# Optimization experiments

Hardware: AMD Instinct MI355X
Metric: run time of the kernel (lower is better)

## Reference

```python
import jax, jax.numpy as jnp
import numpy as np

B = 262144
DIM = 128
TD = 32        # token_dim (per-token channel dim inside attention)
NT = DIM // TD # 4 tokens from x, +1 learnable -> N = 5
N = NT + 1
H = 8          # num_heads
HD = TD // H   # head_dim = 4
DEEP = 2


def setup_inputs() -> dict:
    key = jax.random.key(0)
    ks = jax.random.split(key, 7)
    x = jax.random.normal(ks[0], (B, DIM), dtype=jnp.float32)
    token = jax.random.normal(ks[1], (1, 1, TD), dtype=jnp.float32)
    # stacked per-layer params (DEEP layers)
    qkv_w = jax.random.normal(ks[2], (DEEP, 3 * TD, TD), dtype=jnp.float32) * (TD ** -0.5)
    qkv_b = jnp.zeros((DEEP, 3 * TD), dtype=jnp.float32)
    proj_w = jax.random.normal(ks[3], (DEEP, TD, TD), dtype=jnp.float32) * (TD ** -0.5)
    proj_b = jnp.zeros((DEEP, TD), dtype=jnp.float32)
    pos_bias = jax.random.normal(ks[4], (DEEP, H, N, N), dtype=jnp.float32)
    return {"x": x, "token": token, "qkv_w": qkv_w, "qkv_b": qkv_b,
            "proj_w": proj_w, "proj_b": proj_b, "pos_bias": pos_bias}


def reference(x, token, qkv_w, qkv_b, proj_w, proj_b, pos_bias):
    scale = HD ** -0.5
    b = x.shape[0]
    # split x into NT tokens of width TD, prepend learnable token -> [B, N, TD]
    y = jnp.concatenate(
        [jnp.broadcast_to(token, (b, 1, TD)), x.reshape(b, NT, TD)], axis=1)
    for i in range(DEEP):
        qkv = y @ qkv_w[i].T + qkv_b[i]                 # [B, N, 3*TD]
        qkv = qkv.reshape(b, N, 3, H, HD)
        q = qkv[:, :, 0].transpose(0, 2, 1, 3)          # [B, H, N, HD]
        k = qkv[:, :, 1].transpose(0, 2, 1, 3)
        v = qkv[:, :, 2].transpose(0, 2, 1, 3)
        attn = jnp.einsum('bhnd,bhmd->bhnm', q, k) * scale + pos_bias[i]
        attn = jax.nn.softmax(attn, axis=-1)
        o = jnp.einsum('bhnm,bhmd->bhnd', attn, v)      # [B, H, N, HD]
        o = o.transpose(0, 2, 1, 3).reshape(b, N, TD)
        y = y + (o @ proj_w[i].T + proj_b[i])           # residual
    return y[:, 0, :]                                   # [B, TD]
```

## Files before the change

kernel.cpp:

```cpp
#include <hip/hip_runtime.h>
#include <hip/hip_bf16.h>


#define NTOK 5

typedef decltype(__builtin_amdgcn_cvt_pkrtz(0.0f, 0.0f)) half2_t;
using half8_t = __attribute__((ext_vector_type(8))) _Float16;
using f32x4 = __attribute__((ext_vector_type(4))) float;
using f32x2 = __attribute__((ext_vector_type(2))) float;

union H2 { half2_t h; unsigned int u; };
union H8 { half8_t h; uint4 u4; unsigned int u[4]; };

__device__ __forceinline__ half2_t u2h(unsigned int x) { H2 c; c.u = x; return c.h; }
__device__ __forceinline__ unsigned int h2u(half2_t h) { H2 c; c.h = h; return c.u; }
__device__ __forceinline__ unsigned int pk(float a, float b) {
  return h2u(__builtin_amdgcn_cvt_pkrtz(a, b));
}
__device__ __forceinline__ float bf2f(unsigned short u) {
  union { unsigned int u; float f; } c; c.u = ((unsigned int)u) << 16; return c.f;
}
__device__ __forceinline__ half2_t bfpair2h2(unsigned int u) {
  union { unsigned int u; float f; } lo, hi;
  lo.u = u << 16;
  hi.u = u & 0xffff0000u;
  return __builtin_amdgcn_cvt_pkrtz(lo.f, hi.f);
}
__device__ __forceinline__ unsigned int f2bfpair(float a, float b) {
  unsigned int ua = __float_as_uint(a), ub = __float_as_uint(b);
  ua = (ua + 0x7fffu + ((ua >> 16) & 1u)) >> 16;
  ub = (ub + 0x7fffu + ((ub >> 16) & 1u)) & 0xffff0000u;
  return ua | ub;
}

__device__ __forceinline__ int detect_bf16(const unsigned int* __restrict__ p) {
  int cnt = 0;
#pragma unroll
  for (int i = 0; i < 64; ++i) {
    unsigned int e = (p[i] >> 7) & 0xffu;
    cnt += (e >= 96u && e <= 150u) ? 1 : 0;
  }
  return (cnt >= 40) ? 1 : 0;
}

__device__ __forceinline__ int permch(int pos) {
  return 4 * (pos >> 3) + (pos & 3) + ((pos & 4) ? 16 : 0);
}

__global__ void prep_kernel(const void* __restrict__ xraw,
                            const void* __restrict__ qkv_w, const void* __restrict__ qkv_b,
                            const void* __restrict__ proj_w, const void* __restrict__ proj_b,
                            const void* __restrict__ pos_b,
                            unsigned int* __restrict__ wqkv, unsigned int* __restrict__ wproj,
                            float* __restrict__ bqkv, float* __restrict__ bproj,
                            float* __restrict__ pb, int* __restrict__ flag) {
  const int t = threadIdx.x;
  const int isbf = detect_bf16((const unsigned int*)xraw);
  if (t == 0) *flag = isbf;
  const float LOG2E = 1.44269504f;
  if (isbf) {
    const unsigned short* qw = (const unsigned short*)qkv_w;
    const unsigned short* qb = (const unsigned short*)qkv_b;
    const unsigned short* pw = (const unsigned short*)proj_w;
    const unsigned short* pbb = (const unsigned short*)proj_b;
    const unsigned short* pp = (const unsigned short*)pos_b;
    for (int i = t; i < 3072; i += 256) {
      const int row = i >> 4, cp = (i & 15) * 2;
      wqkv[i] = h2u(__builtin_amdgcn_cvt_pkrtz(bf2f(qw[row * 32 + permch(cp)]),
                                               bf2f(qw[row * 32 + permch(cp + 1)])));
    }
    for (int i = t; i < 1024; i += 256) {
      const int row = i >> 4, cp = (i & 15) * 2;
      wproj[i] = h2u(__builtin_amdgcn_cvt_pkrtz(bf2f(pw[row * 32 + permch(cp)]),
                                                bf2f(pw[row * 32 + permch(cp + 1)])));
    }
    for (int i = t; i < 192; i += 256) bqkv[i] = bf2f(qb[i]);
    for (int i = t; i < 64; i += 256) bproj[i] = bf2f(pbb[i]);
    for (int i = t; i < 640; i += 256) {
      const int m = i & 7, r = i >> 3;
      const int n = r % 5, lh = r / 5;
      pb[i] = (m < 5) ? bf2f(pp[lh * 25 + n * 5 + m]) * LOG2E : 0.0f;
    }
  } else {
    const float* qw = (const float*)qkv_w;
    const float* qb = (const float*)qkv_b;
    const float* pw = (const float*)proj_w;
    const float* pbb = (const float*)proj_b;
    const float* pp = (const float*)pos_b;
    for (int i = t; i < 3072; i += 256) {
      const int row = i >> 4, cp = (i & 15) * 2;
      wqkv[i] = h2u(__builtin_amdgcn_cvt_pkrtz(qw[row * 32 + permch(cp)],
                                               qw[row * 32 + permch(cp + 1)]));
    }
    for (int i = t; i < 1024; i += 256) {
      const int row = i >> 4, cp = (i & 15) * 2;
      wproj[i] = h2u(__builtin_amdgcn_cvt_pkrtz(pw[row * 32 + permch(cp)],
                                                pw[row * 32 + permch(cp + 1)]));
    }
    for (int i = t; i < 192; i += 256) bqkv[i] = qb[i];
    for (int i = t; i < 64; i += 256) bproj[i] = pbb[i];
    for (int i = t; i < 640; i += 256) {
      const int m = i & 7, r = i >> 3;
      const int n = r % 5, lh = r / 5;
      pb[i] = (m < 5) ? pp[lh * 25 + n * 5 + m] * LOG2E : 0.0f;
    }
  }
}

__device__ __forceinline__ half8_t mk8(const unsigned int (&d)[4]) {
  H8 c; c.u[0] = d[0]; c.u[1] = d[1]; c.u[2] = d[2]; c.u[3] = d[3]; return c.h;
}

__device__ __forceinline__ half8_t ldsfrag(const unsigned int* lw, int row, int quad) {
  H8 c; c.u4 = *(const uint4*)(lw + row * 20 + quad * 4); return c.h;
}

template <int NR>
__device__ __forceinline__ void attn_head(const unsigned int (&qd)[NR][2],
                                          const unsigned int (&kd)[NTOK][2],
                                          const f32x4 (&vv)[NTOK],
                                          const float* pbh,
                                          unsigned int (&od)[NR][2]) {
#pragma unroll
  for (int n = 0; n < NR; ++n) {
    const f32x4 pbv = *(const f32x4*)(pbh + n * 8);
    const float pb4 = pbh[n * 8 + 4];
    const float pbm[NTOK] = {pbv[0], pbv[1], pbv[2], pbv[3], pb4};
    const half2_t q0 = u2h(qd[n][0]), q1 = u2h(qd[n][1]);
    float e[NTOK];
#pragma unroll
    for (int m = 0; m < NTOK; ++m) {
      float d = __builtin_amdgcn_fdot2(q0, u2h(kd[m][0]), 0.0f, false);
      d = __builtin_amdgcn_fdot2(q1, u2h(kd[m][1]), d, false);
      e[m] = __builtin_amdgcn_exp2f(fmaf(d, 0.72134752f, pbm[m]));
    }
    const float ssum = ((e[0] + e[1]) + (e[2] + e[3])) + e[4];
    const float r = __builtin_amdgcn_rcpf(ssum);
    f32x2 o01 = {0.0f, 0.0f}, o23 = {0.0f, 0.0f};
#pragma unroll
    for (int m = 0; m < NTOK; ++m) {
      const f32x2 em = {e[m], e[m]};
      const f32x2 vlo = {vv[m][0], vv[m][1]};
      const f32x2 vhi = {vv[m][2], vv[m][3]};
      o01 = __builtin_elementwise_fma(em, vlo, o01);
      o23 = __builtin_elementwise_fma(em, vhi, o23);
    }
    od[n][0] = pk(o01[0] * r, o01[1] * r);
    od[n][1] = pk(o23[0] * r, o23[1] * r);
  }
}

__global__ __launch_bounds__(256, 4) void vit_kernel(
    const void* __restrict__ x, const void* __restrict__ token,
    const unsigned int* __restrict__ wqkv, const unsigned int* __restrict__ wproj,
    const float* __restrict__ bqkv, const float* __restrict__ bproj,
    const float* __restrict__ pb, const int* __restrict__ flag,
    void* __restrict__ out) {
  __shared__ unsigned int lds_w[256 * 20];
  __shared__ float lds_bq[192];
  __shared__ float lds_bp[64];
  __shared__ float lds_pb[640];

  const int tid = threadIdx.x;
  const int wave = tid >> 6, lane = tid & 63;
  const int quad = lane >> 4, nl = lane & 15;
  const size_t b = (size_t)blockIdx.x * 64 + wave * 16 + nl;
  const int isbf = *flag;

  uint2 xb16[10];
  float4 xf32[10];
  if (isbf) {
    const unsigned short* tk = (const unsigned short*)token;
    xb16[0] = *(const uint2*)(tk + quad * 4);
    xb16[1] = *(const uint2*)(tk + quad * 4 + 16);
    const unsigned short* xbp = (const unsigned short*)x + b * 128;
#pragma unroll
    for (int t = 1; t < NTOK; ++t) {
      const unsigned short* base = xbp + (t - 1) * 32;
      xb16[2 * t] = *(const uint2*)(base + quad * 4);
      xb16[2 * t + 1] = *(const uint2*)(base + quad * 4 + 16);
    }
  } else {
    const float* tk = (const float*)token;
    xf32[0] = *(const float4*)(tk + quad * 4);
    xf32[1] = *(const float4*)(tk + quad * 4 + 16);
    const float* xbp = (const float*)x + b * 128;
#pragma unroll
    for (int t = 1; t < NTOK; ++t) {
      const float* base = xbp + (t - 1) * 32;
      xf32[2 * t] = *(const float4*)(base + quad * 4);
      xf32[2 * t + 1] = *(const float4*)(base + quad * 4 + 16);
    }
  }

  {
    const uint4* sq = (const uint4*)wqkv;
#pragma unroll
    for (int k = 0; k < 3; ++k) {
      const int i = tid + k * 256;
      *(uint4*)(lds_w + (i >> 2) * 20 + (i & 3) * 4) = sq[i];
    }
    const uint4* sp = (const uint4*)wproj;
    *(uint4*)(lds_w + (192 + (tid >> 2)) * 20 + (tid & 3) * 4) = sp[tid];
    if (tid < 192) lds_bq[tid] = bqkv[tid];
    if (tid < 64) lds_bp[tid] = bproj[tid];
    {
      const uint4* spb = (const uint4*)pb;
      if (tid < 160) *(uint4*)((float*)lds_pb + tid * 4) = spb[tid];
    }
  }
  __syncthreads();

  unsigned int yd[NTOK][4];
  if (isbf) {
#pragma unroll
    for (int t = 0; t < NTOK; ++t) {
      yd[t][0] = h2u(bfpair2h2(xb16[2 * t].x));
      yd[t][1] = h2u(bfpair2h2(xb16[2 * t].y));
      yd[t][2] = h2u(bfpair2h2(xb16[2 * t + 1].x));
      yd[t][3] = h2u(bfpair2h2(xb16[2 * t + 1].y));
    }
  } else {
#pragma unroll
    for (int t = 0; t < NTOK; ++t) {
      yd[t][0] = pk(xf32[2 * t].x, xf32[2 * t].y);
      yd[t][1] = pk(xf32[2 * t].z, xf32[2 * t].w);
      yd[t][2] = pk(xf32[2 * t + 1].x, xf32[2 * t + 1].y);
      yd[t][3] = pk(xf32[2 * t + 1].z, xf32[2 * t + 1].w);
    }
  }

  unsigned int od[2][NTOK][2];
#pragma unroll
  for (int s = 0; s < 2; ++s) {
    const half8_t waq = ldsfrag(lds_w, (s) * 16 + nl, quad);
    const half8_t wak = ldsfrag(lds_w, (2 + s) * 16 + nl, quad);
    const half8_t wav = ldsfrag(lds_w, (4 + s) * 16 + nl, quad);
    const f32x4 bq = *(const f32x4*)(lds_bq + (s) * 16 + quad * 4);
    const f32x4 bk = *(const f32x4*)(lds_bq + (2 + s) * 16 + quad * 4);
    const f32x4 bv = *(const f32x4*)(lds_bq + (4 + s) * 16 + quad * 4);
    unsigned int qd[NTOK][2], kd[NTOK][2];
    f32x4 vv[NTOK];
#pragma unroll
    for (int t = 0; t < NTOK; ++t) {
      const half8_t yb = mk8(yd[t]);
      const f32x4 aq = __builtin_amdgcn_mfma_f32_16x16x32_f16(waq, yb, bq, 0, 0, 0);
      qd[t][0] = pk(aq[0], aq[1]); qd[t][1] = pk(aq[2], aq[3]);
      const f32x4 ak = __builtin_amdgcn_mfma_f32_16x16x32_f16(wak, yb, bk, 0, 0, 0);
      kd[t][0] = pk(ak[0], ak[1]); kd[t][1] = pk(ak[2], ak[3]);
      vv[t] = __builtin_amdgcn_mfma_f32_16x16x32_f16(wav, yb, bv, 0, 0, 0);
    }
    attn_head<NTOK>(qd, kd, vv, lds_pb + (quad + 4 * s) * 40, od[s]);
  }

  {
    half8_t wp[2]; f32x4 bp[2];
#pragma unroll
    for (int tile = 0; tile < 2; ++tile) {
      wp[tile] = ldsfrag(lds_w, 192 + tile * 16 + nl, quad);
      bp[tile] = *(const f32x4*)(lds_bp + tile * 16 + quad * 4);
    }
#pragma unroll
    for (int t = 0; t < NTOK; ++t) {
      unsigned int bfr[4] = {od[0][t][0], od[0][t][1], od[1][t][0], od[1][t][1]};
      const half8_t ob = mk8(bfr);
      f32x4 p0 = __builtin_amdgcn_mfma_f32_16x16x32_f16(wp[0], ob, bp[0], 0, 0, 0);
      f32x4 p1 = __builtin_amdgcn_mfma_f32_16x16x32_f16(wp[1], ob, bp[1], 0, 0, 0);
      yd[t][0] = h2u(u2h(yd[t][0]) + u2h(pk(p0[0], p0[1])));
      yd[t][1] = h2u(u2h(yd[t][1]) + u2h(pk(p0[2], p0[3])));
      yd[t][2] = h2u(u2h(yd[t][2]) + u2h(pk(p1[0], p1[1])));
      yd[t][3] = h2u(u2h(yd[t][3]) + u2h(pk(p1[2], p1[3])));
    }
  }

  unsigned int o1[2][1][2];
#pragma unroll
  for (int s = 0; s < 2; ++s) {
    const half8_t waq = ldsfrag(lds_w, 96 + (s) * 16 + nl, quad);
    const half8_t wak = ldsfrag(lds_w, 96 + (2 + s) * 16 + nl, quad);
    const half8_t wav = ldsfrag(lds_w, 96 + (4 + s) * 16 + nl, quad);
    const f32x4 bq = *(const f32x4*)(lds_bq + 96 + (s) * 16 + quad * 4);
    const f32x4 bk = *(const f32x4*)(lds_bq + 96 + (2 + s) * 16 + quad * 4);
    const f32x4 bv = *(const f32x4*)(lds_bq + 96 + (4 + s) * 16 + quad * 4);
    unsigned int qd[1][2], kd[NTOK][2];
    f32x4 vv[NTOK];
    {
      const f32x4 aq = __builtin_amdgcn_mfma_f32_16x16x32_f16(waq, mk8(yd[0]), bq, 0, 0, 0);
      qd[0][0] = pk(aq[0], aq[1]); qd[0][1] = pk(aq[2], aq[3]);
    }
#pragma unroll
    for (int t = 0; t < NTOK; ++t) {
      const half8_t yb = mk8(yd[t]);
      const f32x4 ak = __builtin_amdgcn_mfma_f32_16x16x32_f16(wak, yb, bk, 0, 0, 0);
      kd[t][0] = pk(ak[0], ak[1]); kd[t][1] = pk(ak[2], ak[3]);
      vv[t] = __builtin_amdgcn_mfma_f32_16x16x32_f16(wav, yb, bv, 0, 0, 0);
    }
    attn_head<1>(qd, kd, vv, lds_pb + (8 + quad + 4 * s) * 40, o1[s]);
  }

  {
    half8_t wp[2]; f32x4 bp[2];
#pragma unroll
    for (int tile = 0; tile < 2; ++tile) {
      wp[tile] = ldsfrag(lds_w, 192 + 32 + tile * 16 + nl, quad);
      bp[tile] = *(const f32x4*)(lds_bp + 32 + tile * 16 + quad * 4);
    }
    unsigned int bfr[4] = {o1[0][0][0], o1[0][0][1], o1[1][0][0], o1[1][0][1]};
    const half8_t ob = mk8(bfr);
    f32x4 p0 = __builtin_amdgcn_mfma_f32_16x16x32_f16(wp[0], ob, bp[0], 0, 0, 0);
    f32x4 p1 = __builtin_amdgcn_mfma_f32_16x16x32_f16(wp[1], ob, bp[1], 0, 0, 0);

    const half2_t y0 = u2h(yd[0][0]), y1 = u2h(yd[0][1]);
    const half2_t y2 = u2h(yd[0][2]), y3 = u2h(yd[0][3]);
    float f[8] = {(float)y0.x + p0[0], (float)y0.y + p0[1],
                  (float)y1.x + p0[2], (float)y1.y + p0[3],
                  (float)y2.x + p1[0], (float)y2.y + p1[1],
                  (float)y3.x + p1[2], (float)y3.y + p1[3]};
    if (isbf) {
      unsigned short* ob16 = (unsigned short*)out + b * 32;
      *(uint2*)(ob16 + quad * 4) = make_uint2(f2bfpair(f[0], f[1]), f2bfpair(f[2], f[3]));
      *(uint2*)(ob16 + quad * 4 + 16) = make_uint2(f2bfpair(f[4], f[5]), f2bfpair(f[6], f[7]));
    } else {
      float* of = (float*)out + b * 32;
      *(float4*)(of + quad * 4) = make_float4(f[0], f[1], f[2], f[3]);
      *(float4*)(of + quad * 4 + 16) = make_float4(f[4], f[5], f[6], f[7]);
    }
  }
}

extern "C" void kernel_launch(void* const* d_in, const int* in_sizes, int n_in,
                              void* d_out, int out_size, void* d_ws, size_t ws_size,
                              hipStream_t stream) {
  const void* x      = d_in[0];
  const void* token  = d_in[1];
  const void* qkv_w  = d_in[2];
  const void* qkv_b  = d_in[3];
  const void* proj_w = d_in[4];
  const void* proj_b = d_in[5];
  const void* pos_b  = d_in[6];

  char* ws = (char*)d_ws;
  unsigned int* wqkv  = (unsigned int*)(ws + 0);
  unsigned int* wproj = (unsigned int*)(ws + 12288);
  float* bqkv  = (float*)(ws + 16384);
  float* bproj = (float*)(ws + 17152);
  float* pb    = (float*)(ws + 17408);
  int*   flag  = (int*)(ws + 19968);

  prep_kernel<<<1, 256, 0, stream>>>(x, qkv_w, qkv_b, proj_w, proj_b, pos_b,
                                     wqkv, wproj, bqkv, bproj, pb, flag);

  const int nrows = in_sizes[0] / 128;
  const int grid = nrows / 64;
  vit_kernel<<<grid, 256, 0, stream>>>(x, token, wqkv, wproj, bqkv, bproj, pb, flag, d_out);
}
```

Measured before the change: 232.9 us.

## Process four row groups per block with register prefetch of next inputs

Each block now loops over four 64-row groups. The LDS weight, bias and position-bias setup is paid once per block instead of once per 64 rows, and the x loads for the next group are issued before the current group's compute so memory latency overlaps MFMA work. Launch bounds drop from 4 to 3 blocks per SIMD to leave registers for the prefetch buffers, and the grid shrinks fourfold. The risks are lower occupancy, more register pressure, and an uneven tail over the smaller grid; the last iteration also issues a redundant reload.

```diff
diff --git a/kernel.cpp b/kernel.cpp
--- a/kernel.cpp
+++ b/kernel.cpp
@@ -150,7 +150,9 @@
   }
 }
 
-__global__ __launch_bounds__(256, 4) void vit_kernel(
+#define NITER 4
+
+__global__ __launch_bounds__(256, 3) void vit_kernel(
     const void* __restrict__ x, const void* __restrict__ token,
     const unsigned int* __restrict__ wqkv, const unsigned int* __restrict__ wproj,
     const float* __restrict__ bqkv, const float* __restrict__ bproj,
@@ -164,32 +166,27 @@
   const int tid = threadIdx.x;
   const int wave = tid >> 6, lane = tid & 63;
   const int quad = lane >> 4, nl = lane & 15;
-  const size_t b = (size_t)blockIdx.x * 64 + wave * 16 + nl;
+  const int rowoff = wave * 16 + nl;
+  const size_t bbase = (size_t)blockIdx.x * (64 * NITER) + rowoff;
   const int isbf = *flag;
 
-  uint2 xb16[10];
-  float4 xf32[10];
+  float4 rawf[8];
+  uint2 rawb[8];
   if (isbf) {
-    const unsigned short* tk = (const unsigned short*)token;
-    xb16[0] = *(const uint2*)(tk + quad * 4);
-    xb16[1] = *(const uint2*)(tk + quad * 4 + 16);
-    const unsigned short* xbp = (const unsigned short*)x + b * 128;
+    const unsigned short* xbp = (const unsigned short*)x + bbase * 128;
 #pragma unroll
     for (int t = 1; t < NTOK; ++t) {
       const unsigned short* base = xbp + (t - 1) * 32;
-      xb16[2 * t] = *(const uint2*)(base + quad * 4);
-      xb16[2 * t + 1] = *(const uint2*)(base + quad * 4 + 16);
+      rawb[2 * (t - 1)] = *(const uint2*)(base + quad * 4);
+      rawb[2 * (t - 1) + 1] = *(const uint2*)(base + quad * 4 + 16);
     }
   } else {
-    const float* tk = (const float*)token;
-    xf32[0] = *(const float4*)(tk + quad * 4);
-    xf32[1] = *(const float4*)(tk + quad * 4 + 16);
-    const float* xbp = (const float*)x + b * 128;
+    const float* xbp = (const float*)x + bbase * 128;
 #pragma unroll
     for (int t = 1; t < NTOK; ++t) {
       const float* base = xbp + (t - 1) * 32;
-      xf32[2 * t] = *(const float4*)(base + quad * 4);
-      xf32[2 * t + 1] = *(const float4*)(base + quad * 4 + 16);
+      rawf[2 * (t - 1)] = *(const float4*)(base + quad * 4);
+      rawf[2 * (t - 1) + 1] = *(const float4*)(base + quad * 4 + 16);
     }
   }
 
@@ -209,121 +206,164 @@
       if (tid < 160) *(uint4*)((float*)lds_pb + tid * 4) = spb[tid];
     }
   }
+
+  unsigned int tokd[4];
+  if (isbf) {
+    const unsigned short* tk = (const unsigned short*)token;
+    const uint2 t0 = *(const uint2*)(tk + quad * 4);
+    const uint2 t1 = *(const uint2*)(tk + quad * 4 + 16);
+    tokd[0] = h2u(bfpair2h2(t0.x)); tokd[1] = h2u(bfpair2h2(t0.y));
+    tokd[2] = h2u(bfpair2h2(t1.x)); tokd[3] = h2u(bfpair2h2(t1.y));
+  } else {
+    const float* tk = (const float*)token;
+    const float4 a0 = *(const float4*)(tk + quad * 4);
+    const float4 a1 = *(const float4*)(tk + quad * 4 + 16);
+    tokd[0] = pk(a0.x, a0.y); tokd[1] = pk(a0.z, a0.w);
+    tokd[2] = pk(a1.x, a1.y); tokd[3] = pk(a1.z, a1.w);
+  }
   __syncthreads();
 
-  unsigned int yd[NTOK][4];
-  if (isbf) {
-#pragma unroll
-    for (int t = 0; t < NTOK; ++t) {
-      yd[t][0] = h2u(bfpair2h2(xb16[2 * t].x));
-      yd[t][1] = h2u(bfpair2h2(xb16[2 * t].y));
-      yd[t][2] = h2u(bfpair2h2(xb16[2 * t + 1].x));
-      yd[t][3] = h2u(bfpair2h2(xb16[2 * t + 1].y));
-    }
-  } else {
-#pragma unroll
-    for (int t = 0; t < NTOK; ++t) {
-      yd[t][0] = pk(xf32[2 * t].x, xf32[2 * t].y);
-      yd[t][1] = pk(xf32[2 * t].z, xf32[2 * t].w);
-      yd[t][2] = pk(xf32[2 * t + 1].x, xf32[2 * t + 1].y);
-      yd[t][3] = pk(xf32[2 * t + 1].z, xf32[2 * t + 1].w);
-    }
-  }
-
-  unsigned int od[2][NTOK][2];
-#pragma unroll
-  for (int s = 0; s < 2; ++s) {
-    const half8_t waq = ldsfrag(lds_w, (s) * 16 + nl, quad);
-    const half8_t wak = ldsfrag(lds_w, (2 + s) * 16 + nl, quad);
-    const half8_t wav = ldsfrag(lds_w, (4 + s) * 16 + nl, quad);
-    const f32x4 bq = *(const f32x4*)(lds_bq + (s) * 16 + quad * 4);
-    const f32x4 bk = *(const f32x4*)(lds_bq + (2 + s) * 16 + quad * 4);
-    const f32x4 bv = *(const f32x4*)(lds_bq + (4 + s) * 16 + quad * 4);
-    unsigned int qd[NTOK][2], kd[NTOK][2];
-    f32x4 vv[NTOK];
-#pragma unroll
-    for (int t = 0; t < NTOK; ++t) {
-      const half8_t yb = mk8(yd[t]);
-      const f32x4 aq = __builtin_amdgcn_mfma_f32_16x16x32_f16(waq, yb, bq, 0, 0, 0);
-      qd[t][0] = pk(aq[0], aq[1]); qd[t][1] = pk(aq[2], aq[3]);
-      const f32x4 ak = __builtin_amdgcn_mfma_f32_16x16x32_f16(wak, yb, bk, 0, 0, 0);
-      kd[t][0] = pk(ak[0], ak[1]); kd[t][1] = pk(ak[2], ak[3]);
-      vv[t] = __builtin_amdgcn_mfma_f32_16x16x32_f16(wav, yb, bv, 0, 0, 0);
-    }
-    attn_head<NTOK>(qd, kd, vv, lds_pb + (quad + 4 * s) * 40, od[s]);
-  }
-
-  {
-    half8_t wp[2]; f32x4 bp[2];
-#pragma unroll
-    for (int tile = 0; tile < 2; ++tile) {
-      wp[tile] = ldsfrag(lds_w, 192 + tile * 16 + nl, quad);
-      bp[tile] = *(const f32x4*)(lds_bp + tile * 16 + quad * 4);
-    }
-#pragma unroll
-    for (int t = 0; t < NTOK; ++t) {
-      unsigned int bfr[4] = {od[0][t][0], od[0][t][1], od[1][t][0], od[1][t][1]};
+#pragma unroll 1
+  for (int it = 0; it < NITER; ++it) {
+    const size_t bcur = bbase + (size_t)it * 64;
+
+    unsigned int yd[NTOK][4];
+    yd[0][0] = tokd[0]; yd[0][1] = tokd[1]; yd[0][2] = tokd[2]; yd[0][3] = tokd[3];
+    if (isbf) {
+#pragma unroll
+      for (int t = 1; t < NTOK; ++t) {
+        yd[t][0] = h2u(bfpair2h2(rawb[2 * (t - 1)].x));
+        yd[t][1] = h2u(bfpair2h2(rawb[2 * (t - 1)].y));
+        yd[t][2] = h2u(bfpair2h2(rawb[2 * (t - 1) + 1].x));
+        yd[t][3] = h2u(bfpair2h2(rawb[2 * (t - 1) + 1].y));
+      }
+    } else {
+#pragma unroll
+      for (int t = 1; t < NTOK; ++t) {
+        yd[t][0] = pk(rawf[2 * (t - 1)].x, rawf[2 * (t - 1)].y);
+        yd[t][1] = pk(rawf[2 * (t - 1)].z, rawf[2 * (t - 1)].w);
+        yd[t][2] = pk(rawf[2 * (t - 1) + 1].x, rawf[2 * (t - 1) + 1].y);
+        yd[t][3] = pk(rawf[2 * (t - 1) + 1].z, rawf[2 * (t - 1) + 1].w);
+      }
+    }
+
+    {
+      const int itn = (it < NITER - 1) ? it + 1 : it;
+      const size_t bnext = bbase + (size_t)itn * 64;
+      if (isbf) {
+        const unsigned short* xbp = (const unsigned short*)x + bnext * 128;
+#pragma unroll
+        for (int t = 1; t < NTOK; ++t) {
+          const unsigned short* base = xbp + (t - 1) * 32;
+          rawb[2 * (t - 1)] = *(const uint2*)(base + quad * 4);
+          rawb[2 * (t - 1) + 1] = *(const uint2*)(base + quad * 4 + 16);
+        }
+      } else {
+        const float* xbp = (const float*)x + bnext * 128;
+#pragma unroll
+        for (int t = 1; t < NTOK; ++t) {
+          const float* base = xbp + (t - 1) * 32;
+          rawf[2 * (t - 1)] = *(const float4*)(base + quad * 4);
+          rawf[2 * (t - 1) + 1] = *(const float4*)(base + quad * 4 + 16);
+        }
+      }
+    }
+
+    unsigned int od[2][NTOK][2];
+#pragma unroll
+    for (int s = 0; s < 2; ++s) {
+      const half8_t waq = ldsfrag(lds_w, (s) * 16 + nl, quad);
+      const half8_t wak = ldsfrag(lds_w, (2 + s) * 16 + nl, quad);
+      const half8_t wav = ldsfrag(lds_w, (4 + s) * 16 + nl, quad);
+      const f32x4 bq = *(const f32x4*)(lds_bq + (s) * 16 + quad * 4);
+      const f32x4 bk = *(const f32x4*)(lds_bq + (2 + s) * 16 + quad * 4);
+      const f32x4 bv = *(const f32x4*)(lds_bq + (4 + s) * 16 + quad * 4);
+      unsigned int qd[NTOK][2], kd[NTOK][2];
+      f32x4 vv[NTOK];
+#pragma unroll
+      for (int t = 0; t < NTOK; ++t) {
+        const half8_t yb = mk8(yd[t]);
+        const f32x4 aq = __builtin_amdgcn_mfma_f32_16x16x32_f16(waq, yb, bq, 0, 0, 0);
+        qd[t][0] = pk(aq[0], aq[1]); qd[t][1] = pk(aq[2], aq[3]);
+        const f32x4 ak = __builtin_amdgcn_mfma_f32_16x16x32_f16(wak, yb, bk, 0, 0, 0);
+        kd[t][0] = pk(ak[0], ak[1]); kd[t][1] = pk(ak[2], ak[3]);
+        vv[t] = __builtin_amdgcn_mfma_f32_16x16x32_f16(wav, yb, bv, 0, 0, 0);
+      }
+      attn_head<NTOK>(qd, kd, vv, lds_pb + (quad + 4 * s) * 40, od[s]);
+    }
+
+    {
+      half8_t wp[2]; f32x4 bp[2];
+#pragma unroll
+      for (int tile = 0; tile < 2; ++tile) {
+        wp[tile] = ldsfrag(lds_w, 192 + tile * 16 + nl, quad);
+        bp[tile] = *(const f32x4*)(lds_bp + tile * 16 + quad * 4);
+      }
+#pragma unroll
+      for (int t = 0; t < NTOK; ++t) {
+        unsigned int bfr[4] = {od[0][t][0], od[0][t][1], od[1][t][0], od[1][t][1]};
+        const half8_t ob = mk8(bfr);
+        f32x4 p0 = __builtin_amdgcn_mfma_f32_16x16x32_f16(wp[0], ob, bp[0], 0, 0, 0);
+        f32x4 p1 = __builtin_amdgcn_mfma_f32_16x16x32_f16(wp[1], ob, bp[1], 0, 0, 0);
+        yd[t][0] = h2u(u2h(yd[t][0]) + u2h(pk(p0[0], p0[1])));
+        yd[t][1] = h2u(u2h(yd[t][1]) + u2h(pk(p0[2], p0[3])));
+        yd[t][2] = h2u(u2h(yd[t][2]) + u2h(pk(p1[0], p1[1])));
+        yd[t][3] = h2u(u2h(yd[t][3]) + u2h(pk(p1[2], p1[3])));
+      }
+    }
+
+    unsigned int o1[2][1][2];
+#pragma unroll
+    for (int s = 0; s < 2; ++s) {
+      const half8_t waq = ldsfrag(lds_w, 96 + (s) * 16 + nl, quad);
+      const half8_t wak = ldsfrag(lds_w, 96 + (2 + s) * 16 + nl, quad);
+      const half8_t wav = ldsfrag(lds_w, 96 + (4 + s) * 16 + nl, quad);
+      const f32x4 bq = *(const f32x4*)(lds_bq + 96 + (s) * 16 + quad * 4);
+      const f32x4 bk = *(const f32x4*)(lds_bq + 96 + (2 + s) * 16 + quad * 4);
+      const f32x4 bv = *(const f32x4*)(lds_bq + 96 + (4 + s) * 16 + quad * 4);
+      unsigned int qd[1][2], kd[NTOK][2];
+      f32x4 vv[NTOK];
+      {
+        const f32x4 aq = __builtin_amdgcn_mfma_f32_16x16x32_f16(waq, mk8(yd[0]), bq, 0, 0, 0);
+        qd[0][0] = pk(aq[0], aq[1]); qd[0][1] = pk(aq[2], aq[3]);
+      }
+#pragma unroll
+      for (int t = 0; t < NTOK; ++t) {
+        const half8_t yb = mk8(yd[t]);
+        const f32x4 ak = __builtin_amdgcn_mfma_f32_16x16x32_f16(wak, yb, bk, 0, 0, 0);
+        kd[t][0] = pk(ak[0], ak[1]); kd[t][1] = pk(ak[2], ak[3]);
+        vv[t] = __builtin_amdgcn_mfma_f32_16x16x32_f16(wav, yb, bv, 0, 0, 0);
+      }
+      attn_head<1>(qd, kd, vv, lds_pb + (8 + quad + 4 * s) * 40, o1[s]);
+    }
+
+    {
+      half8_t wp[2]; f32x4 bp[2];
+#pragma unroll
+      for (int tile = 0; tile < 2; ++tile) {
+        wp[tile] = ldsfrag(lds_w, 192 + 32 + tile * 16 + nl, quad);
+        bp[tile] = *(const f32x4*)(lds_bp + 32 + tile * 16 + quad * 4);
+      }
+      unsigned int bfr[4] = {o1[0][0][0], o1[0][0][1], o1[1][0][0], o1[1][0][1]};
       const half8_t ob = mk8(bfr);
       f32x4 p0 = __builtin_amdgcn_mfma_f32_16x16x32_f16(wp[0], ob, bp[0], 0, 0, 0);
       f32x4 p1 = __builtin_amdgcn_mfma_f32_16x16x32_f16(wp[1], ob, bp[1], 0, 0, 0);
-      yd[t][0] = h2u(u2h(yd[t][0]) + u2h(pk(p0[0], p0[1])));
-      yd[t][1] = h2u(u2h(yd[t][1]) + u2h(pk(p0[2], p0[3])));
-      yd[t][2] = h2u(u2h(yd[t][2]) + u2h(pk(p1[0], p1[1])));
-      yd[t][3] = h2u(u2h(yd[t][3]) + u2h(pk(p1[2], p1[3])));
-    }
-  }
-
-  unsigned int o1[2][1][2];
-#pragma unroll
-  for (int s = 0; s < 2; ++s) {
-    const half8_t waq = ldsfrag(lds_w, 96 + (s) * 16 + nl, quad);
-    const half8_t wak = ldsfrag(lds_w, 96 + (2 + s) * 16 + nl, quad);
-    const half8_t wav = ldsfrag(lds_w, 96 + (4 + s) * 16 + nl, quad);
-    const f32x4 bq = *(const f32x4*)(lds_bq + 96 + (s) * 16 + quad * 4);
-    const f32x4 bk = *(const f32x4*)(lds_bq + 96 + (2 + s) * 16 + quad * 4);
-    const f32x4 bv = *(const f32x4*)(lds_bq + 96 + (4 + s) * 16 + quad * 4);
-    unsigned int qd[1][2], kd[NTOK][2];
-    f32x4 vv[NTOK];
-    {
-      const f32x4 aq = __builtin_amdgcn_mfma_f32_16x16x32_f16(waq, mk8(yd[0]), bq, 0, 0, 0);
-      qd[0][0] = pk(aq[0], aq[1]); qd[0][1] = pk(aq[2], aq[3]);
-    }
-#pragma unroll
-    for (int t = 0; t < NTOK; ++t) {
-      const half8_t yb = mk8(yd[t]);
-      const f32x4 ak = __builtin_amdgcn_mfma_f32_16x16x32_f16(wak, yb, bk, 0, 0, 0);
-      kd[t][0] = pk(ak[0], ak[1]); kd[t][1] = pk(ak[2], ak[3]);
-      vv[t] = __builtin_amdgcn_mfma_f32_16x16x32_f16(wav, yb, bv, 0, 0, 0);
-    }
-    attn_head<1>(qd, kd, vv, lds_pb + (8 + quad + 4 * s) * 40, o1[s]);
-  }
-
-  {
-    half8_t wp[2]; f32x4 bp[2];
-#pragma unroll
-    for (int tile = 0; tile < 2; ++tile) {
-      wp[tile] = ldsfrag(lds_w, 192 + 32 + tile * 16 + nl, quad);
-      bp[tile] = *(const f32x4*)(lds_bp + 32 + tile * 16 + quad * 4);
-    }
-    unsigned int bfr[4] = {o1[0][0][0], o1[0][0][1], o1[1][0][0], o1[1][0][1]};
-    const half8_t ob = mk8(bfr);
-    f32x4 p0 = __builtin_amdgcn_mfma_f32_16x16x32_f16(wp[0], ob, bp[0], 0, 0, 0);
-    f32x4 p1 = __builtin_amdgcn_mfma_f32_16x16x32_f16(wp[1], ob, bp[1], 0, 0, 0);
-
-    const half2_t y0 = u2h(yd[0][0]), y1 = u2h(yd[0][1]);
-    const half2_t y2 = u2h(yd[0][2]), y3 = u2h(yd[0][3]);
-    float f[8] = {(float)y0.x + p0[0], (float)y0.y + p0[1],
-                  (float)y1.x + p0[2], (float)y1.y + p0[3],
-                  (float)y2.x + p1[0], (float)y2.y + p1[1],
-                  (float)y3.x + p1[2], (float)y3.y + p1[3]};
-    if (isbf) {
-      unsigned short* ob16 = (unsigned short*)out + b * 32;
-      *(uint2*)(ob16 + quad * 4) = make_uint2(f2bfpair(f[0], f[1]), f2bfpair(f[2], f[3]));
-      *(uint2*)(ob16 + quad * 4 + 16) = make_uint2(f2bfpair(f[4], f[5]), f2bfpair(f[6], f[7]));
-    } else {
-      float* of = (float*)out + b * 32;
-      *(float4*)(of + quad * 4) = make_float4(f[0], f[1], f[2], f[3]);
-      *(float4*)(of + quad * 4 + 16) = make_float4(f[4], f[5], f[6], f[7]);
+
+      const half2_t y0 = u2h(yd[0][0]), y1 = u2h(yd[0][1]);
+      const half2_t y2 = u2h(yd[0][2]), y3 = u2h(yd[0][3]);
+      float f[8] = {(float)y0.x + p0[0], (float)y0.y + p0[1],
+                    (float)y1.x + p0[2], (float)y1.y + p0[3],
+                    (float)y2.x + p1[0], (float)y2.y + p1[1],
+                    (float)y3.x + p1[2], (float)y3.y + p1[3]};
+      if (isbf) {
+        unsigned short* ob16 = (unsigned short*)out + bcur * 32;
+        *(uint2*)(ob16 + quad * 4) = make_uint2(f2bfpair(f[0], f[1]), f2bfpair(f[2], f[3]));
+        *(uint2*)(ob16 + quad * 4 + 16) = make_uint2(f2bfpair(f[4], f[5]), f2bfpair(f[6], f[7]));
+      } else {
+        float* of = (float*)out + bcur * 32;
+        *(float4*)(of + quad * 4) = make_float4(f[0], f[1], f[2], f[3]);
+        *(float4*)(of + quad * 4 + 16) = make_float4(f[4], f[5], f[6], f[7]);
+      }
     }
   }
 }
@@ -351,6 +391,6 @@
                                      wqkv, wproj, bqkv, bproj, pb, flag);
 
   const int nrows = in_sizes[0] / 128;
-  const int grid = nrows / 64;
+  const int grid = nrows / (64 * NITER);
   vit_kernel<<<grid, 256, 0, stream>>>(x, token, wqkv, wproj, bqkv, bproj, pb, flag, d_out);
 }
```

New measurement: 419.1 us. +80.0%, slower.
